# Performance work log

Hardware: AMD Instinct MI355X
Metric: run time of the kernel (lower is better)

## Reference

```python
import math
import jax, jax.numpy as jnp
import numpy as np

N = 50000       # num_nodes
D = 128         # input feature dim
OUT = 128       # output_dim
H = 8           # num_heads
F = OUT // H    # out_feats per head (= self_attn hidden_dim)
E_RAND = 800000 # random edges per graph (+ N self loops)
ALPHA = 0.8
BETA = 0.5


def _edges(key):
    k1, k2 = jax.random.split(key)
    src = jax.random.randint(k1, (E_RAND,), 0, N, dtype=jnp.int32)
    dst = jax.random.randint(k2, (E_RAND,), 0, N, dtype=jnp.int32)
    loop = jnp.arange(N, dtype=jnp.int32)  # dgl.add_self_loop
    return jnp.concatenate([src, loop]), jnp.concatenate([dst, loop])


def setup_inputs() -> dict:
    key = jax.random.key(0)
    ks = jax.random.split(key, 32)
    inp = {"x": jax.random.normal(ks[0], (N, D), jnp.float32)}
    inp["src_s"], inp["dst_s"] = _edges(ks[1])
    inp["src_t"], inp["dst_t"] = _edges(ks[2])
    inp["src_p"], inp["dst_p"] = _edges(ks[3])
    i = 4
    for v in ("s", "t", "p"):
        inp[f"W_{v}"] = jax.random.normal(ks[i], (OUT, D), jnp.float32) * 0.05; i += 1
        inp[f"al_{v}"] = jax.random.normal(ks[i], (H, F), jnp.float32) * 0.1; i += 1
        inp[f"ar_{v}"] = jax.random.normal(ks[i], (H, F), jnp.float32) * 0.1; i += 1
        inp[f"b_{v}"] = jnp.zeros((OUT,), jnp.float32)
    inp["Wq"] = jax.random.normal(ks[i], (F, OUT), jnp.float32) * 0.05; i += 1
    inp["bq"] = jnp.zeros((F,), jnp.float32)
    inp["Wk"] = jax.random.normal(ks[i], (F, OUT), jnp.float32) * 0.05; i += 1
    inp["bk"] = jnp.zeros((F,), jnp.float32)
    inp["Wm"] = jax.random.normal(ks[i], (1, N * OUT), jnp.float32) * 0.001; i += 1
    inp["bm"] = jnp.zeros((1,), jnp.float32)
    return inp


def _gat(x, src, dst, W, al, ar, b):
    # DGL GATConv (eval mode, negative_slope=0.2, activation=relu)
    feat = (x @ W.T).reshape(N, H, F)                      # [N,H,F]
    el = jnp.einsum('nhf,hf->nh', feat, al)                # [N,H]
    er = jnp.einsum('nhf,hf->nh', feat, ar)
    e = jax.nn.leaky_relu(el[src] + er[dst], 0.2)          # [E,H]
    m = jax.ops.segment_max(e, dst, num_segments=N)        # per-dst softmax
    ex = jnp.exp(e - m[dst])
    s = jax.ops.segment_sum(ex, dst, num_segments=N)
    attn = ex / s[dst]                                     # [E,H]
    out = jax.ops.segment_sum(feat[src] * attn[:, :, None], dst, num_segments=N)
    return jax.nn.relu(out + b.reshape(1, H, F)).reshape(N, OUT)


def reference(x, src_s, dst_s, src_t, dst_t, src_p, dst_p,
              W_s, al_s, ar_s, b_s, W_t, al_t, ar_t, b_t,
              W_p, al_p, ar_p, b_p, Wq, bq, Wk, bk, Wm, bm):
    s = _gat(x, src_s, dst_s, W_s, al_s, ar_s, b_s)
    t = _gat(x, src_t, dst_t, W_t, al_t, ar_t, b_t)
    p = _gat(x, src_p, dst_p, W_p, al_p, ar_p, b_p)
    views = jnp.stack([s, t, p])                           # [3,N,OUT]
    # self_attn: one scalar attention weight per view
    Q = jnp.einsum('vne,he->vnh', views, Wq) + bq          # [3,N,F]
    K = jnp.einsum('vne,he->vnh', views, Wk) + bk
    logits = jnp.sum(Q.reshape(3, -1) * K.reshape(3, -1), -1) / math.sqrt(F * N)
    w = jax.nn.softmax(logits)                             # [3]
    fused = w[:, None, None] * views
    views2 = ALPHA * fused + (1.0 - ALPHA) * views         # [3,N,OUT]
    # mv_attn: sigmoid-gated sum of views
    omega = jax.nn.sigmoid(views2.reshape(3, -1) @ Wm.T + bm)[:, 0]  # [3]
    mv = jnp.einsum('v,vne->ne', omega, views2)            # [N,OUT]
    result = BETA * views2 + (1.0 - BETA) * mv[None]       # [3,N,OUT]
    return mv, result
```

## Files before the change

kernel.cpp:

```cpp
#include <hip/hip_runtime.h>


#define N_NODES 50000
#define DIM 128
#define OUTD 128
#define NH 8
#define NF 16
#define NE 850000
#define NOFF 50001
#define NBUCK 49
#define BCAP 20480
#define BIN_EPT 8
#define BIN_EPB 2048

typedef float f32x4 __attribute__((ext_vector_type(4)));
typedef float f32x2 __attribute__((ext_vector_type(2)));
typedef __bf16 bf16x8 __attribute__((ext_vector_type(8)));
typedef unsigned short u16x8 __attribute__((ext_vector_type(8)));

static __device__ __forceinline__ float bf2f_lo(unsigned int u) {
  return __uint_as_float(u << 16);
}
static __device__ __forceinline__ float bf2f_hi(unsigned int u) {
  return __uint_as_float(u & 0xffff0000u);
}
static __device__ __forceinline__ f32x2 up2(unsigned int u) {
  f32x2 r;
  r.x = __uint_as_float(u << 16);
  r.y = __uint_as_float(u & 0xffff0000u);
  return r;
}
static __device__ __forceinline__ unsigned short f2bf(float f) {
  unsigned int u = __float_as_uint(f);
  unsigned int r = (u + 0x7fffu + ((u >> 16) & 1u)) >> 16;
  return (unsigned short)r;
}

__global__ __launch_bounds__(256) void gemm_feat_kernel(
    const float* __restrict__ x, const float* __restrict__ Ws,
    const float* __restrict__ Wt, const float* __restrict__ Wp,
    unsigned short* __restrict__ feat) {
  __shared__ unsigned short xa[128 * 128];
  __shared__ unsigned short wb[128 * 128];
  const int t = threadIdx.x;
  const int n0 = blockIdx.x * 128;

  for (int i = 0; i < 16; ++i) {
    int flat = (i * 256 + t) * 4;
    int r = flat >> 7, c = flat & 127;
    float4 val = make_float4(0.f, 0.f, 0.f, 0.f);
    if (n0 + r < N_NODES) val = *(const float4*)(x + (size_t)(n0 + r) * DIM + c);
    int byteoff = (r * 256 + c * 2) ^ ((r & 7) << 4);
    unsigned short* p = (unsigned short*)((char*)xa + byteoff);
    p[0] = f2bf(val.x); p[1] = f2bf(val.y); p[2] = f2bf(val.z); p[3] = f2bf(val.w);
  }

  const int wave = t >> 6, lane = t & 63;
  const int wr = wave >> 1, wc = wave & 1;
  const int lrow = lane & 15;
  const int kgrp = lane >> 4;

  for (int v = 0; v < 3; ++v) {
    const float* W = (v == 0) ? Ws : ((v == 1) ? Wt : Wp);
    __syncthreads();
    for (int i = 0; i < 16; ++i) {
      int flat = (i * 256 + t) * 4;
      int r = flat >> 7, c = flat & 127;
      float4 val = *(const float4*)(W + r * DIM + c);
      int byteoff = (r * 256 + c * 2) ^ ((r & 7) << 4);
      unsigned short* p = (unsigned short*)((char*)wb + byteoff);
      p[0] = f2bf(val.x); p[1] = f2bf(val.y); p[2] = f2bf(val.z); p[3] = f2bf(val.w);
    }
    __syncthreads();

    f32x4 acc[4][4];
    for (int m = 0; m < 4; ++m)
      for (int n = 0; n < 4; ++n) acc[m][n] = (f32x4)0.f;

    for (int ks = 0; ks < 4; ++ks) {
      bf16x8 af[4], bfr[4];
      int kb2 = (ks * 32 + kgrp * 8) * 2;
      for (int m = 0; m < 4; ++m) {
        int r = wr * 64 + m * 16 + lrow;
        af[m] = *(const bf16x8*)((const char*)xa + ((r * 256 + kb2) ^ ((r & 7) << 4)));
      }
      for (int n = 0; n < 4; ++n) {
        int r = wc * 64 + n * 16 + lrow;
        bfr[n] = *(const bf16x8*)((const char*)wb + ((r * 256 + kb2) ^ ((r & 7) << 4)));
      }
      for (int m = 0; m < 4; ++m)
        for (int n = 0; n < 4; ++n)
          acc[m][n] = __builtin_amdgcn_mfma_f32_16x16x32_bf16(af[m], bfr[n], acc[m][n], 0, 0, 0);
    }

    unsigned short* fv = feat + (size_t)v * N_NODES * OUTD;
    for (int m = 0; m < 4; ++m)
      for (int n = 0; n < 4; ++n) {
        int col = wc * 64 + n * 16 + lrow;
        for (int r4 = 0; r4 < 4; ++r4) {
          int row = n0 + wr * 64 + m * 16 + kgrp * 4 + r4;
          if (row < N_NODES) fv[(size_t)row * OUTD + col] = f2bf(acc[m][n][r4]);
        }
      }
  }
}

__global__ __launch_bounds__(256) void elr_kernel(
    const unsigned short* __restrict__ feat,
    const float* __restrict__ al_s, const float* __restrict__ ar_s,
    const float* __restrict__ al_t, const float* __restrict__ ar_t,
    const float* __restrict__ al_p, const float* __restrict__ ar_p,
    float* __restrict__ el, float* __restrict__ er) {
  int idx = blockIdx.x * 256 + threadIdx.x;
  if (idx >= 3 * N_NODES * NH) return;
  int v = idx / (N_NODES * NH);
  int rem = idx - v * (N_NODES * NH);
  int n = rem >> 3, h = rem & 7;
  const float* al = (v == 0) ? al_s : ((v == 1) ? al_t : al_p);
  const float* ar = (v == 0) ? ar_s : ((v == 1) ? ar_t : ar_p);
  const unsigned short* fr = feat + (size_t)v * N_NODES * OUTD + (size_t)n * OUTD + h * NF;
  uint4 a = *(const uint4*)(fr);
  uint4 b = *(const uint4*)(fr + 8);
  float fv[16];
  fv[0] = bf2f_lo(a.x); fv[1] = bf2f_hi(a.x); fv[2] = bf2f_lo(a.y); fv[3] = bf2f_hi(a.y);
  fv[4] = bf2f_lo(a.z); fv[5] = bf2f_hi(a.z); fv[6] = bf2f_lo(a.w); fv[7] = bf2f_hi(a.w);
  fv[8] = bf2f_lo(b.x); fv[9] = bf2f_hi(b.x); fv[10] = bf2f_lo(b.y); fv[11] = bf2f_hi(b.y);
  fv[12] = bf2f_lo(b.z); fv[13] = bf2f_hi(b.z); fv[14] = bf2f_lo(b.w); fv[15] = bf2f_hi(b.w);
  float accl = 0.f, accr = 0.f;
#pragma unroll
  for (int f = 0; f < NF; ++f) {
    accl += fv[f] * al[h * NF + f];
    accr += fv[f] * ar[h * NF + f];
  }
  el[idx] = accl;
  er[idx] = accr;
}

__global__ __launch_bounds__(256) void bin_kernel(
    const int* __restrict__ src_s, const int* __restrict__ dst_s,
    const int* __restrict__ src_t, const int* __restrict__ dst_t,
    const int* __restrict__ src_p, const int* __restrict__ dst_p,
    int* __restrict__ gtail, unsigned int* __restrict__ gbin) {
  const int v = blockIdx.y;
  const int* S = (v == 0) ? src_s : ((v == 1) ? src_t : src_p);
  const int* D = (v == 0) ? dst_s : ((v == 1) ? dst_t : dst_p);
  __shared__ int lhist[4][64], lbase[4][64];
  const int t = threadIdx.x;
  const int wave = t >> 6;
  ((int*)lhist)[t] = 0;
  __syncthreads();
  const int e0 = blockIdx.x * BIN_EPB + t * BIN_EPT;
  unsigned int pk[BIN_EPT];
  int bk[BIN_EPT], rk[BIN_EPT];
#pragma unroll
  for (int i = 0; i < BIN_EPT; ++i) {
    int e = e0 + i;
    if (e < NE) {
      unsigned int s = (unsigned int)S[e], d = (unsigned int)D[e];
      pk[i] = (s << 16) | d;
      bk[i] = (int)(d >> 10);
      rk[i] = atomicAdd(&lhist[wave][bk[i]], 1);
    } else {
      bk[i] = -1;
    }
  }
  __syncthreads();
  if (t < 64) {
    int c0 = lhist[0][t], c1 = lhist[1][t], c2 = lhist[2][t], c3 = lhist[3][t];
    int tot = c0 + c1 + c2 + c3;
    int gb = (tot > 0) ? atomicAdd(&gtail[v * 64 + t], tot) : 0;
    lbase[0][t] = gb;
    lbase[1][t] = gb + c0;
    lbase[2][t] = gb + c0 + c1;
    lbase[3][t] = gb + c0 + c1 + c2;
  }
  __syncthreads();
#pragma unroll
  for (int i = 0; i < BIN_EPT; ++i) {
    if (bk[i] >= 0) {
      int pos = lbase[wave][bk[i]] + rk[i];
      if (pos < BCAP)
        gbin[((size_t)v * 64 + bk[i]) * BCAP + pos] = pk[i];
    }
  }
}

__global__ __launch_bounds__(1024) void bucket_sort_kernel(
    const int* __restrict__ gtail, const unsigned int* __restrict__ gbin,
    int* __restrict__ offs, int* __restrict__ esrc) {
  __shared__ int lcur[1024];
  __shared__ int wsum[16];
  __shared__ int sh_bbase;
  __shared__ unsigned int sorted[BCAP];
  __shared__ int lhist[1024];
  const int v = blockIdx.y;
  const int b = blockIdx.x;
  const int t = threadIdx.x;
  const int wave = t >> 6, lane = t & 63;

  int cnt = gtail[v * 64 + b];
  if (cnt > BCAP) cnt = BCAP;
  const unsigned int* eb = gbin + ((size_t)v * 64 + b) * BCAP;

  if (t < 64) {
    int valb = (t < b) ? gtail[v * 64 + t] : 0;
#pragma unroll
    for (int m = 1; m < 64; m <<= 1) valb += __shfl_xor(valb, m, 64);
    if (t == 0) sh_bbase = valb;
  }
  lhist[t] = 0;
  __syncthreads();

  for (int e = t; e < cnt; e += 1024)
    atomicAdd(&lhist[eb[e] & 1023u], 1);
  __syncthreads();

  int val = lhist[t];
  int incl = val;
#pragma unroll
  for (int st = 1; st < 64; st <<= 1) {
    int o = __shfl_up(incl, st, 64);
    if (lane >= st) incl += o;
  }
  if (lane == 63) wsum[wave] = incl;
  __syncthreads();
  if (t < 64) {
    int wv = (lane < 16) ? wsum[lane] : 0;
    int winc = wv;
#pragma unroll
    for (int st = 1; st < 16; st <<= 1) {
      int o = __shfl_up(winc, st, 64);
      if (lane >= st) winc += o;
    }
    if (lane < 16) wsum[lane] = winc - wv;
  }
  __syncthreads();
  const int base = wsum[wave] + incl - val;
  lcur[t] = base;

  const int bbase = sh_bbase;
  if (b == 0 && t == 0) offs[v * NOFF] = 0;
  {
    int n = b * 1024 + t;
    if (n < N_NODES) offs[v * NOFF + n + 1] = bbase + base + val;
  }
  __syncthreads();

  for (int e = t; e < cnt; e += 1024) {
    unsigned int pk = eb[e];
    int pos = atomicAdd(&lcur[pk & 1023u], 1);
    sorted[pos] = pk >> 16;
  }
  __syncthreads();

  int* ev = esrc + (size_t)v * NE + bbase;
  for (int e = t; e < cnt; e += 1024) ev[e] = (int)sorted[e];
}

__global__ __launch_bounds__(256) void gat_kernel(
    const int* __restrict__ offs, const int* __restrict__ esrc,
    const float* __restrict__ el, const float* __restrict__ er,
    const unsigned short* __restrict__ feat,
    const float* __restrict__ b_s, const float* __restrict__ b_t,
    const float* __restrict__ b_p, float* __restrict__ views) {
  const int v = blockIdx.y;
  const int n = blockIdx.x * 4 + (threadIdx.x >> 6);
  const int lane = threadIdx.x & 63;
  const int g = lane >> 4;
  const int q = lane & 15;
  const int h = q >> 1;
  const int* off_v = offs + v * NOFF;
  const int off0 = off_v[n];
  const int deg = off_v[n + 1] - off0;
  const int* es = esrc + (size_t)v * NE + off0;
  const float* el_v = el + (size_t)v * N_NODES * NH;
  const float er_h = er[((size_t)v * N_NODES + n) * NH + h];
  const unsigned short* featv = feat + (size_t)v * N_NODES * OUTD;

  f32x2 acc2[4];
#pragma unroll
  for (int j = 0; j < 4; ++j) acc2[j] = (f32x2)0.f;
  float sm = 0.f;

  int e0 = g, e1 = 4 + g;
  bool v0 = e0 < deg, v1 = e1 < deg;
  int s0 = es[v0 ? e0 : 0];
  int s1 = es[v1 ? e1 : 0];
  float l0 = el_v[s0 * NH + h];
  float l1 = el_v[s1 * NH + h];
  uint4 pk0 = *(const uint4*)(featv + (size_t)s0 * OUTD + q * 8);
  uint4 pk1 = *(const uint4*)(featv + (size_t)s1 * OUTD + q * 8);

  for (int base = 0; base < deg; base += 8) {
    bool cv0 = v0, cv1 = v1;
    float cl0 = l0, cl1 = l1;
    uint4 cp0 = pk0, cp1 = pk1;
    int nb = base + 8;
    if (nb < deg) {
      e0 = nb + g; e1 = nb + 4 + g;
      v0 = e0 < deg; v1 = e1 < deg;
      s0 = es[v0 ? e0 : 0];
      s1 = es[v1 ? e1 : 0];
      l0 = el_v[s0 * NH + h];
      l1 = el_v[s1 * NH + h];
      pk0 = *(const uint4*)(featv + (size_t)s0 * OUTD + q * 8);
      pk1 = *(const uint4*)(featv + (size_t)s1 * OUTD + q * 8);
    }
    float val0 = cl0 + er_h;
    float val1 = cl1 + er_h;
    val0 = fmaxf(val0, 0.2f * val0);
    val1 = fmaxf(val1, 0.2f * val1);
    float aw0 = cv0 ? __expf(val0) : 0.f;
    float aw1 = cv1 ? __expf(val1) : 0.f;
    sm += aw0 + aw1;
    acc2[0] += aw0 * up2(cp0.x) + aw1 * up2(cp1.x);
    acc2[1] += aw0 * up2(cp0.y) + aw1 * up2(cp1.y);
    acc2[2] += aw0 * up2(cp0.z) + aw1 * up2(cp1.z);
    acc2[3] += aw0 * up2(cp0.w) + aw1 * up2(cp1.w);
  }

#pragma unroll
  for (int m = 16; m < 64; m <<= 1) {
    sm += __shfl_xor(sm, m, 64);
#pragma unroll
    for (int j = 0; j < 4; ++j) {
      acc2[j].x += __shfl_xor(acc2[j].x, m, 64);
      acc2[j].y += __shfl_xor(acc2[j].y, m, 64);
    }
  }

  if (g == 0) {
    const float inv = 1.0f / sm;
    const float* bv = (v == 0) ? b_s : ((v == 1) ? b_t : b_p);
    float r[8];
#pragma unroll
    for (int j = 0; j < 4; ++j) {
      float x0 = acc2[j].x * inv + bv[q * 8 + 2 * j];
      float x1 = acc2[j].y * inv + bv[q * 8 + 2 * j + 1];
      r[2 * j] = (x0 > 0.f) ? x0 : 0.f;
      r[2 * j + 1] = (x1 > 0.f) ? x1 : 0.f;
    }
    float* dst = views + (size_t)v * N_NODES * OUTD + (size_t)n * OUTD + q * 8;
    *(float4*)(dst) = make_float4(r[0], r[1], r[2], r[3]);
    *(float4*)(dst + 4) = make_float4(r[4], r[5], r[6], r[7]);
  }
}

__global__ __launch_bounds__(256) void viewred_kernel(
    const float* __restrict__ views, const float* __restrict__ Wq,
    const float* __restrict__ bq, const float* __restrict__ Wk,
    const float* __restrict__ bk, const float* __restrict__ Wm,
    float* __restrict__ logits, float* __restrict__ dsum) {
  __shared__ unsigned short vt[128 * 128];
  __shared__ unsigned short wq[16 * 128];
  __shared__ unsigned short wk[16 * 128];
  __shared__ float redq[4], redd[4];
  const int n0 = blockIdx.x * 128;
  const int t = threadIdx.x;
  const int wave = t >> 6, lane = t & 63;
  const int lrow = lane & 15;
  const int kgrp = lane >> 4;

  {
    int flat = t * 8;
    int r = flat >> 7, c = flat & 127;
    int byteoff = (r * 256 + c * 2) ^ ((r & 7) << 4);
    float4 qa = *(const float4*)(Wq + flat);
    float4 qb = *(const float4*)(Wq + flat + 4);
    u16x8 oq;
    oq[0] = f2bf(qa.x); oq[1] = f2bf(qa.y); oq[2] = f2bf(qa.z); oq[3] = f2bf(qa.w);
    oq[4] = f2bf(qb.x); oq[5] = f2bf(qb.y); oq[6] = f2bf(qb.z); oq[7] = f2bf(qb.w);
    *(u16x8*)((char*)wq + byteoff) = oq;
    float4 ka = *(const float4*)(Wk + flat);
    float4 kb = *(const float4*)(Wk + flat + 4);
    u16x8 ok;
    ok[0] = f2bf(ka.x); ok[1] = f2bf(ka.y); ok[2] = f2bf(ka.z); ok[3] = f2bf(ka.w);
    ok[4] = f2bf(kb.x); ok[5] = f2bf(kb.y); ok[6] = f2bf(kb.z); ok[7] = f2bf(kb.w);
    *(u16x8*)((char*)wk + byteoff) = ok;
  }

  const float bqv = bq[lrow];
  const float bkv = bk[lrow];

  for (int v = 0; v < 3; ++v) {
    const float* Vv = views + (size_t)v * N_NODES * OUTD;
    float dp = 0.f;
    for (int i = 0; i < 8; ++i) {
      int flat = (i * 256 + t) * 8;
      int r = flat >> 7, c = flat & 127;
      int row = n0 + r;
      u16x8 o = (u16x8)0;
      if (row < N_NODES) {
        size_t goff = (size_t)row * OUTD + c;
        float4 a = *(const float4*)(Vv + goff);
        float4 b = *(const float4*)(Vv + goff + 4);
        float4 wa = *(const float4*)(Wm + goff);
        float4 wb2 = *(const float4*)(Wm + goff + 4);
        dp += a.x * wa.x + a.y * wa.y + a.z * wa.z + a.w * wa.w;
        dp += b.x * wb2.x + b.y * wb2.y + b.z * wb2.z + b.w * wb2.w;
        o[0] = f2bf(a.x); o[1] = f2bf(a.y); o[2] = f2bf(a.z); o[3] = f2bf(a.w);
        o[4] = f2bf(b.x); o[5] = f2bf(b.y); o[6] = f2bf(b.z); o[7] = f2bf(b.w);
      }
      int byteoff = (r * 256 + c * 2) ^ ((r & 7) << 4);
      *(u16x8*)((char*)vt + byteoff) = o;
    }
    __syncthreads();

    float qk = 0.f;
    f32x4 accQ[2], accK[2];
    accQ[0] = (f32x4)0.f; accQ[1] = (f32x4)0.f;
    accK[0] = (f32x4)0.f; accK[1] = (f32x4)0.f;
    for (int ks = 0; ks < 4; ++ks) {
      int kb2 = (ks * 32 + kgrp * 8) * 2;
      int rb = lrow;
      bf16x8 bqf = *(const bf16x8*)((const char*)wq + ((rb * 256 + kb2) ^ ((rb & 7) << 4)));
      bf16x8 bkf = *(const bf16x8*)((const char*)wk + ((rb * 256 + kb2) ^ ((rb & 7) << 4)));
#pragma unroll
      for (int m = 0; m < 2; ++m) {
        int r = (wave * 2 + m) * 16 + lrow;
        bf16x8 af = *(const bf16x8*)((const char*)vt + ((r * 256 + kb2) ^ ((r & 7) << 4)));
        accQ[m] = __builtin_amdgcn_mfma_f32_16x16x32_bf16(af, bqf, accQ[m], 0, 0, 0);
        accK[m] = __builtin_amdgcn_mfma_f32_16x16x32_bf16(af, bkf, accK[m], 0, 0, 0);
      }
    }
#pragma unroll
    for (int m = 0; m < 2; ++m) {
#pragma unroll
      for (int j = 0; j < 4; ++j) {
        int row = n0 + (wave * 2 + m) * 16 + kgrp * 4 + j;
        if (row < N_NODES) qk += (accQ[m][j] + bqv) * (accK[m][j] + bkv);
      }
    }

#pragma unroll
    for (int m = 1; m < 64; m <<= 1) {
      qk += __shfl_xor(qk, m, 64);
      dp += __shfl_xor(dp, m, 64);
    }
    if (lane == 0) { redq[wave] = qk; redd[wave] = dp; }
    __syncthreads();
    if (t == 0) {
      atomicAdd(&logits[v], redq[0] + redq[1] + redq[2] + redq[3]);
      atomicAdd(&dsum[v], redd[0] + redd[1] + redd[2] + redd[3]);
    }
    __syncthreads();
  }
}

__global__ void scalar_kernel(const float* __restrict__ logits,
                              const float* __restrict__ dsum,
                              const float* __restrict__ bm, float* __restrict__ gc) {
  if (threadIdx.x == 0 && blockIdx.x == 0) {
    const float scale = 1.0f / sqrtf((float)(NF * N_NODES));
    float l0 = logits[0] * scale, l1 = logits[1] * scale, l2 = logits[2] * scale;
    float mx = fmaxf(l0, fmaxf(l1, l2));
    float e0 = __expf(l0 - mx), e1 = __expf(l1 - mx), e2 = __expf(l2 - mx);
    float inv = 1.0f / (e0 + e1 + e2);
    float g0 = 0.8f * e0 * inv + 0.2f;
    float g1 = 0.8f * e1 * inv + 0.2f;
    float g2 = 0.8f * e2 * inv + 0.2f;
    float bmv = bm[0];
    float o0 = 1.0f / (1.0f + __expf(-(g0 * dsum[0] + bmv)));
    float o1 = 1.0f / (1.0f + __expf(-(g1 * dsum[1] + bmv)));
    float o2 = 1.0f / (1.0f + __expf(-(g2 * dsum[2] + bmv)));
    gc[0] = g0; gc[1] = g1; gc[2] = g2;
    gc[3] = o0 * g0; gc[4] = o1 * g1; gc[5] = o2 * g2;
  }
}

__global__ __launch_bounds__(256) void final_kernel(
    const float* __restrict__ views, const float* __restrict__ gc,
    float* __restrict__ out) {
  const size_t NT = (size_t)N_NODES * OUTD;
  size_t base = ((size_t)blockIdx.x * 256 + threadIdx.x) * 4;
  if (base >= NT) return;
  float g0 = gc[0], g1 = gc[1], g2 = gc[2], c0 = gc[3], c1 = gc[4], c2 = gc[5];
  float4 a0 = *(const float4*)(views + base);
  float4 a1 = *(const float4*)(views + NT + base);
  float4 a2 = *(const float4*)(views + 2 * NT + base);
  float4 mv;
  mv.x = c0 * a0.x + c1 * a1.x + c2 * a2.x;
  mv.y = c0 * a0.y + c1 * a1.y + c2 * a2.y;
  mv.z = c0 * a0.z + c1 * a1.z + c2 * a2.z;
  mv.w = c0 * a0.w + c1 * a1.w + c2 * a2.w;
  *(float4*)(out + base) = mv;
  float4 r;
  r.x = 0.5f * (g0 * a0.x) + 0.5f * mv.x;
  r.y = 0.5f * (g0 * a0.y) + 0.5f * mv.y;
  r.z = 0.5f * (g0 * a0.z) + 0.5f * mv.z;
  r.w = 0.5f * (g0 * a0.w) + 0.5f * mv.w;
  *(float4*)(out + NT + base) = r;
  r.x = 0.5f * (g1 * a1.x) + 0.5f * mv.x;
  r.y = 0.5f * (g1 * a1.y) + 0.5f * mv.y;
  r.z = 0.5f * (g1 * a1.z) + 0.5f * mv.z;
  r.w = 0.5f * (g1 * a1.w) + 0.5f * mv.w;
  *(float4*)(out + 2 * NT + base) = r;
  r.x = 0.5f * (g2 * a2.x) + 0.5f * mv.x;
  r.y = 0.5f * (g2 * a2.y) + 0.5f * mv.y;
  r.z = 0.5f * (g2 * a2.z) + 0.5f * mv.z;
  r.w = 0.5f * (g2 * a2.w) + 0.5f * mv.w;
  *(float4*)(out + 3 * NT + base) = r;
}

extern "C" void kernel_launch(void* const* d_in, const int* in_sizes, int n_in,
                              void* d_out, int out_size, void* d_ws, size_t ws_size,
                              hipStream_t stream) {
  const float* x = (const float*)d_in[0];
  const int* src_s = (const int*)d_in[1];
  const int* dst_s = (const int*)d_in[2];
  const int* src_t = (const int*)d_in[3];
  const int* dst_t = (const int*)d_in[4];
  const int* src_p = (const int*)d_in[5];
  const int* dst_p = (const int*)d_in[6];
  const float* W_s = (const float*)d_in[7];
  const float* al_s = (const float*)d_in[8];
  const float* ar_s = (const float*)d_in[9];
  const float* b_s = (const float*)d_in[10];
  const float* W_t = (const float*)d_in[11];
  const float* al_t = (const float*)d_in[12];
  const float* ar_t = (const float*)d_in[13];
  const float* b_t = (const float*)d_in[14];
  const float* W_p = (const float*)d_in[15];
  const float* al_p = (const float*)d_in[16];
  const float* ar_p = (const float*)d_in[17];
  const float* b_p = (const float*)d_in[18];
  const float* Wq = (const float*)d_in[19];
  const float* bq = (const float*)d_in[20];
  const float* Wk = (const float*)d_in[21];
  const float* bk = (const float*)d_in[22];
  const float* Wm = (const float*)d_in[23];
  const float* bm = (const float*)d_in[24];
  float* out = (float*)d_out;

  char* ws = (char*)d_ws;
  unsigned short* feat = (unsigned short*)ws;
  float* el = (float*)(ws + 38400000);
  float* er = (float*)(ws + 43200000);
  float* views = (float*)(ws + 48000000);
  int* offs = (int*)(ws + 124800000);
  int* esrc = (int*)(ws + 126000016);
  int* gtail = (int*)(ws + 136800016);
  float* scal = (float*)(ws + 136800784);

  unsigned int* gbin = (unsigned int*)(ws + 49000000);

  hipMemsetAsync(gtail, 0, 768 + 48, stream);

  gemm_feat_kernel<<<dim3(391), dim3(256), 0, stream>>>(x, W_s, W_t, W_p, feat);
  elr_kernel<<<dim3((3 * N_NODES * NH + 255) / 256), dim3(256), 0, stream>>>(
      feat, al_s, ar_s, al_t, ar_t, al_p, ar_p, el, er);
  bin_kernel<<<dim3((NE + BIN_EPB - 1) / BIN_EPB, 3), dim3(256), 0, stream>>>(
      src_s, dst_s, src_t, dst_t, src_p, dst_p, gtail, gbin);
  bucket_sort_kernel<<<dim3(NBUCK, 3), dim3(1024), 0, stream>>>(
      gtail, gbin, offs, esrc);
  gat_kernel<<<dim3(12500, 3), dim3(256), 0, stream>>>(
      offs, esrc, el, er, feat, b_s, b_t, b_p, views);
  viewred_kernel<<<dim3(391), dim3(256), 0, stream>>>(
      views, Wq, bq, Wk, bk, Wm, scal, scal + 3);
  scalar_kernel<<<dim3(1), dim3(64), 0, stream>>>(scal, scal + 3, bm, scal + 6);
  final_kernel<<<dim3(6250), dim3(256), 0, stream>>>(views, scal + 6, out);
}
```

Before: 418.9 us.

## Fuse attention-score projection into GEMM, finer dst buckets, split view grid

The feature GEMM now runs one view per blockIdx.y and stages its bf16 tile in shared memory. From there it writes coalesced feat rows and computes el/er directly, so the separate elr kernel and its re-read of feat are gone. Edge binning uses 256-node buckets (196 buckets) with a separate scan kernel for bucket bases, and bucket sort scatters straight to global memory instead of staging in shared memory. The view-reduction kernel uses 64-row tiles with twice the blocks to raise parallelism. Smaller buckets could overflow BCAP under skewed degree distributions, and direct global scatter gives less coalesced writes.

```diff
diff --git a/kernel.cpp b/kernel.cpp
--- a/kernel.cpp
+++ b/kernel.cpp
@@ -8,10 +8,10 @@
 #define NF 16
 #define NE 850000
 #define NOFF 50001
-#define NBUCK 49
-#define BCAP 20480
-#define BIN_EPT 8
-#define BIN_EPB 2048
+#define NBUCK 196
+#define BCAP 5120
+#define BIN_EPT 16
+#define BIN_EPB 4096
 
 typedef float f32x4 __attribute__((ext_vector_type(4)));
 typedef float f32x2 __attribute__((ext_vector_type(2)));
@@ -20,9 +20,6 @@
 
 static __device__ __forceinline__ float bf2f_lo(unsigned int u) {
   return __uint_as_float(u << 16);
-}
-static __device__ __forceinline__ float bf2f_hi(unsigned int u) {
-  return __uint_as_float(u & 0xffff0000u);
 }
 static __device__ __forceinline__ f32x2 up2(unsigned int u) {
   f32x2 r;
@@ -39,11 +36,20 @@
 __global__ __launch_bounds__(256) void gemm_feat_kernel(
     const float* __restrict__ x, const float* __restrict__ Ws,
     const float* __restrict__ Wt, const float* __restrict__ Wp,
-    unsigned short* __restrict__ feat) {
+    const float* __restrict__ al_s, const float* __restrict__ ar_s,
+    const float* __restrict__ al_t, const float* __restrict__ ar_t,
+    const float* __restrict__ al_p, const float* __restrict__ ar_p,
+    unsigned short* __restrict__ feat, float* __restrict__ el,
+    float* __restrict__ er) {
   __shared__ unsigned short xa[128 * 128];
   __shared__ unsigned short wb[128 * 128];
+  __shared__ float alS[128], arS[128];
   const int t = threadIdx.x;
   const int n0 = blockIdx.x * 128;
+  const int v = blockIdx.y;
+  const float* W = (v == 0) ? Ws : ((v == 1) ? Wt : Wp);
+  const float* alv = (v == 0) ? al_s : ((v == 1) ? al_t : al_p);
+  const float* arv = (v == 0) ? ar_s : ((v == 1) ? ar_t : ar_p);
 
   for (int i = 0; i < 16; ++i) {
     int flat = (i * 256 + t) * 4;
@@ -54,86 +60,90 @@
     unsigned short* p = (unsigned short*)((char*)xa + byteoff);
     p[0] = f2bf(val.x); p[1] = f2bf(val.y); p[2] = f2bf(val.z); p[3] = f2bf(val.w);
   }
+  for (int i = 0; i < 16; ++i) {
+    int flat = (i * 256 + t) * 4;
+    int r = flat >> 7, c = flat & 127;
+    float4 val = *(const float4*)(W + r * DIM + c);
+    int byteoff = (r * 256 + c * 2) ^ ((r & 7) << 4);
+    unsigned short* p = (unsigned short*)((char*)wb + byteoff);
+    p[0] = f2bf(val.x); p[1] = f2bf(val.y); p[2] = f2bf(val.z); p[3] = f2bf(val.w);
+  }
+  if (t < 128) alS[t] = alv[t];
+  else arS[t - 128] = arv[t - 128];
+  __syncthreads();
 
   const int wave = t >> 6, lane = t & 63;
   const int wr = wave >> 1, wc = wave & 1;
   const int lrow = lane & 15;
   const int kgrp = lane >> 4;
-
-  for (int v = 0; v < 3; ++v) {
-    const float* W = (v == 0) ? Ws : ((v == 1) ? Wt : Wp);
-    __syncthreads();
-    for (int i = 0; i < 16; ++i) {
-      int flat = (i * 256 + t) * 4;
-      int r = flat >> 7, c = flat & 127;
-      float4 val = *(const float4*)(W + r * DIM + c);
-      int byteoff = (r * 256 + c * 2) ^ ((r & 7) << 4);
-      unsigned short* p = (unsigned short*)((char*)wb + byteoff);
-      p[0] = f2bf(val.x); p[1] = f2bf(val.y); p[2] = f2bf(val.z); p[3] = f2bf(val.w);
-    }
-    __syncthreads();
-
-    f32x4 acc[4][4];
+  const int row = t >> 1, half = t & 1;
+  const int grow = n0 + row;
+
+  f32x4 acc[4][4];
+  for (int m = 0; m < 4; ++m)
+    for (int n = 0; n < 4; ++n) acc[m][n] = (f32x4)0.f;
+
+  for (int ks = 0; ks < 4; ++ks) {
+    bf16x8 af[4], bfr[4];
+    int kb2 = (ks * 32 + kgrp * 8) * 2;
+    for (int m = 0; m < 4; ++m) {
+      int r = wr * 64 + m * 16 + lrow;
+      af[m] = *(const bf16x8*)((const char*)xa + ((r * 256 + kb2) ^ ((r & 7) << 4)));
+    }
+    for (int n = 0; n < 4; ++n) {
+      int r = wc * 64 + n * 16 + lrow;
+      bfr[n] = *(const bf16x8*)((const char*)wb + ((r * 256 + kb2) ^ ((r & 7) << 4)));
+    }
     for (int m = 0; m < 4; ++m)
-      for (int n = 0; n < 4; ++n) acc[m][n] = (f32x4)0.f;
-
-    for (int ks = 0; ks < 4; ++ks) {
-      bf16x8 af[4], bfr[4];
-      int kb2 = (ks * 32 + kgrp * 8) * 2;
-      for (int m = 0; m < 4; ++m) {
-        int r = wr * 64 + m * 16 + lrow;
-        af[m] = *(const bf16x8*)((const char*)xa + ((r * 256 + kb2) ^ ((r & 7) << 4)));
+      for (int n = 0; n < 4; ++n)
+        acc[m][n] = __builtin_amdgcn_mfma_f32_16x16x32_bf16(af[m], bfr[n], acc[m][n], 0, 0, 0);
+  }
+
+  __syncthreads();
+  for (int m = 0; m < 4; ++m)
+    for (int n = 0; n < 4; ++n) {
+      int col = wc * 64 + n * 16 + lrow;
+#pragma unroll
+      for (int r4 = 0; r4 < 4; ++r4) {
+        int r = wr * 64 + m * 16 + kgrp * 4 + r4;
+        int bo = (r * 256 + col * 2) ^ ((r & 7) << 4);
+        *(unsigned short*)((char*)wb + bo) = f2bf(acc[m][n][r4]);
       }
-      for (int n = 0; n < 4; ++n) {
-        int r = wc * 64 + n * 16 + lrow;
-        bfr[n] = *(const bf16x8*)((const char*)wb + ((r * 256 + kb2) ^ ((r & 7) << 4)));
+    }
+  __syncthreads();
+
+  unsigned short* fv = feat + (size_t)v * N_NODES * OUTD;
+  if (grow < N_NODES) {
+    const int cb = half * 64;
+#pragma unroll
+    for (int i = 0; i < 8; ++i) {
+      int c = cb + i * 8;
+      u16x8 val = *(const u16x8*)((const char*)wb + ((row * 256 + c * 2) ^ ((row & 7) << 4)));
+      *(u16x8*)(fv + (size_t)grow * OUTD + c) = val;
+    }
+    float4 elq, erq;
+    float* elp = (float*)&elq;
+    float* erp = (float*)&erq;
+#pragma unroll
+    for (int k = 0; k < 4; ++k) {
+      int h = half * 4 + k;
+      int c = h * 16;
+      u16x8 f0 = *(const u16x8*)((const char*)wb + ((row * 256 + c * 2) ^ ((row & 7) << 4)));
+      u16x8 f1 = *(const u16x8*)((const char*)wb + ((row * 256 + (c + 8) * 2) ^ ((row & 7) << 4)));
+      float accl = 0.f, accr = 0.f;
+#pragma unroll
+      for (int f = 0; f < 8; ++f) {
+        float v0 = bf2f_lo((unsigned int)(unsigned short)f0[f]);
+        float v1 = bf2f_lo((unsigned int)(unsigned short)f1[f]);
+        accl += v0 * alS[c + f] + v1 * alS[c + 8 + f];
+        accr += v0 * arS[c + f] + v1 * arS[c + 8 + f];
       }
-      for (int m = 0; m < 4; ++m)
-        for (int n = 0; n < 4; ++n)
-          acc[m][n] = __builtin_amdgcn_mfma_f32_16x16x32_bf16(af[m], bfr[n], acc[m][n], 0, 0, 0);
-    }
-
-    unsigned short* fv = feat + (size_t)v * N_NODES * OUTD;
-    for (int m = 0; m < 4; ++m)
-      for (int n = 0; n < 4; ++n) {
-        int col = wc * 64 + n * 16 + lrow;
-        for (int r4 = 0; r4 < 4; ++r4) {
-          int row = n0 + wr * 64 + m * 16 + kgrp * 4 + r4;
-          if (row < N_NODES) fv[(size_t)row * OUTD + col] = f2bf(acc[m][n][r4]);
-        }
-      }
-  }
-}
-
-__global__ __launch_bounds__(256) void elr_kernel(
-    const unsigned short* __restrict__ feat,
-    const float* __restrict__ al_s, const float* __restrict__ ar_s,
-    const float* __restrict__ al_t, const float* __restrict__ ar_t,
-    const float* __restrict__ al_p, const float* __restrict__ ar_p,
-    float* __restrict__ el, float* __restrict__ er) {
-  int idx = blockIdx.x * 256 + threadIdx.x;
-  if (idx >= 3 * N_NODES * NH) return;
-  int v = idx / (N_NODES * NH);
-  int rem = idx - v * (N_NODES * NH);
-  int n = rem >> 3, h = rem & 7;
-  const float* al = (v == 0) ? al_s : ((v == 1) ? al_t : al_p);
-  const float* ar = (v == 0) ? ar_s : ((v == 1) ? ar_t : ar_p);
-  const unsigned short* fr = feat + (size_t)v * N_NODES * OUTD + (size_t)n * OUTD + h * NF;
-  uint4 a = *(const uint4*)(fr);
-  uint4 b = *(const uint4*)(fr + 8);
-  float fv[16];
-  fv[0] = bf2f_lo(a.x); fv[1] = bf2f_hi(a.x); fv[2] = bf2f_lo(a.y); fv[3] = bf2f_hi(a.y);
-  fv[4] = bf2f_lo(a.z); fv[5] = bf2f_hi(a.z); fv[6] = bf2f_lo(a.w); fv[7] = bf2f_hi(a.w);
-  fv[8] = bf2f_lo(b.x); fv[9] = bf2f_hi(b.x); fv[10] = bf2f_lo(b.y); fv[11] = bf2f_hi(b.y);
-  fv[12] = bf2f_lo(b.z); fv[13] = bf2f_hi(b.z); fv[14] = bf2f_lo(b.w); fv[15] = bf2f_hi(b.w);
-  float accl = 0.f, accr = 0.f;
-#pragma unroll
-  for (int f = 0; f < NF; ++f) {
-    accl += fv[f] * al[h * NF + f];
-    accr += fv[f] * ar[h * NF + f];
-  }
-  el[idx] = accl;
-  er[idx] = accr;
+      elp[k] = accl; erp[k] = accr;
+    }
+    size_t eo = ((size_t)v * N_NODES + n0) * NH + t * 4;
+    *(float4*)(el + eo) = elq;
+    *(float4*)(er + eo) = erq;
+  }
 }
 
 __global__ __launch_bounds__(256) void bin_kernel(
@@ -144,31 +154,32 @@
   const int v = blockIdx.y;
   const int* S = (v == 0) ? src_s : ((v == 1) ? src_t : src_p);
   const int* D = (v == 0) ? dst_s : ((v == 1) ? dst_t : dst_p);
-  __shared__ int lhist[4][64], lbase[4][64];
+  __shared__ int lhist[4][256], lbase[4][256];
   const int t = threadIdx.x;
   const int wave = t >> 6;
-  ((int*)lhist)[t] = 0;
+#pragma unroll
+  for (int i = 0; i < 4; ++i) ((int*)lhist)[i * 256 + t] = 0;
   __syncthreads();
   const int e0 = blockIdx.x * BIN_EPB + t * BIN_EPT;
   unsigned int pk[BIN_EPT];
-  int bk[BIN_EPT], rk[BIN_EPT];
+  short bk[BIN_EPT], rk[BIN_EPT];
 #pragma unroll
   for (int i = 0; i < BIN_EPT; ++i) {
     int e = e0 + i;
     if (e < NE) {
       unsigned int s = (unsigned int)S[e], d = (unsigned int)D[e];
       pk[i] = (s << 16) | d;
-      bk[i] = (int)(d >> 10);
-      rk[i] = atomicAdd(&lhist[wave][bk[i]], 1);
+      bk[i] = (short)(d >> 8);
+      rk[i] = (short)atomicAdd(&lhist[wave][bk[i]], 1);
     } else {
       bk[i] = -1;
     }
   }
   __syncthreads();
-  if (t < 64) {
+  {
     int c0 = lhist[0][t], c1 = lhist[1][t], c2 = lhist[2][t], c3 = lhist[3][t];
     int tot = c0 + c1 + c2 + c3;
-    int gb = (tot > 0) ? atomicAdd(&gtail[v * 64 + t], tot) : 0;
+    int gb = (tot > 0) ? atomicAdd(&gtail[v * 256 + t], tot) : 0;
     lbase[0][t] = gb;
     lbase[1][t] = gb + c0;
     lbase[2][t] = gb + c0 + c1;
@@ -180,39 +191,58 @@
     if (bk[i] >= 0) {
       int pos = lbase[wave][bk[i]] + rk[i];
       if (pos < BCAP)
-        gbin[((size_t)v * 64 + bk[i]) * BCAP + pos] = pk[i];
-    }
-  }
-}
-
-__global__ __launch_bounds__(1024) void bucket_sort_kernel(
-    const int* __restrict__ gtail, const unsigned int* __restrict__ gbin,
+        gbin[((size_t)v * 256 + bk[i]) * BCAP + pos] = pk[i];
+    }
+  }
+}
+
+__global__ __launch_bounds__(256) void bscan_kernel(
+    const int* __restrict__ gtail, int* __restrict__ gbase) {
+  __shared__ int wsum[4];
+  const int t = threadIdx.x;
+  const int wave = t >> 6, lane = t & 63;
+  for (int v = 0; v < 3; ++v) {
+    int val = gtail[v * 256 + t];
+    if (val > BCAP) val = BCAP;
+    if (t >= NBUCK) val = 0;
+    int incl = val;
+#pragma unroll
+    for (int st = 1; st < 64; st <<= 1) {
+      int o = __shfl_up(incl, st, 64);
+      if (lane >= st) incl += o;
+    }
+    if (lane == 63) wsum[wave] = incl;
+    __syncthreads();
+    int wb = 0;
+#pragma unroll
+    for (int i = 0; i < 4; ++i) wb += (i < wave) ? wsum[i] : 0;
+    gbase[v * 256 + t] = wb + incl - val;
+    __syncthreads();
+  }
+}
+
+__global__ __launch_bounds__(256) void bucket_sort_kernel(
+    const int* __restrict__ gtail, const int* __restrict__ gbase,
+    const unsigned int* __restrict__ gbin,
     int* __restrict__ offs, int* __restrict__ esrc) {
-  __shared__ int lcur[1024];
-  __shared__ int wsum[16];
-  __shared__ int sh_bbase;
-  __shared__ unsigned int sorted[BCAP];
-  __shared__ int lhist[1024];
+  __shared__ int lhist[256];
+  __shared__ int lcur[256];
+  __shared__ int wsum[4];
   const int v = blockIdx.y;
   const int b = blockIdx.x;
   const int t = threadIdx.x;
   const int wave = t >> 6, lane = t & 63;
 
-  int cnt = gtail[v * 64 + b];
+  int cnt = gtail[v * 256 + b];
   if (cnt > BCAP) cnt = BCAP;
-  const unsigned int* eb = gbin + ((size_t)v * 64 + b) * BCAP;
-
-  if (t < 64) {
-    int valb = (t < b) ? gtail[v * 64 + t] : 0;
-#pragma unroll
-    for (int m = 1; m < 64; m <<= 1) valb += __shfl_xor(valb, m, 64);
-    if (t == 0) sh_bbase = valb;
-  }
+  const unsigned int* eb = gbin + ((size_t)v * 256 + b) * BCAP;
+  const int bbase = gbase[v * 256 + b];
+
   lhist[t] = 0;
   __syncthreads();
 
-  for (int e = t; e < cnt; e += 1024)
-    atomicAdd(&lhist[eb[e] & 1023u], 1);
+  for (int e = t; e < cnt; e += 256)
+    atomicAdd(&lhist[eb[e] & 255u], 1);
   __syncthreads();
 
   int val = lhist[t];
@@ -224,37 +254,25 @@
   }
   if (lane == 63) wsum[wave] = incl;
   __syncthreads();
-  if (t < 64) {
-    int wv = (lane < 16) ? wsum[lane] : 0;
-    int winc = wv;
-#pragma unroll
-    for (int st = 1; st < 16; st <<= 1) {
-      int o = __shfl_up(winc, st, 64);
-      if (lane >= st) winc += o;
-    }
-    if (lane < 16) wsum[lane] = winc - wv;
-  }
-  __syncthreads();
-  const int base = wsum[wave] + incl - val;
-  lcur[t] = base;
-
-  const int bbase = sh_bbase;
+  int wb = 0;
+#pragma unroll
+  for (int i = 0; i < 4; ++i) wb += (i < wave) ? wsum[i] : 0;
+  const int base = wb + incl - val;
+  lcur[t] = bbase + base;
+
   if (b == 0 && t == 0) offs[v * NOFF] = 0;
   {
-    int n = b * 1024 + t;
+    int n = b * 256 + t;
     if (n < N_NODES) offs[v * NOFF + n + 1] = bbase + base + val;
   }
   __syncthreads();
 
-  for (int e = t; e < cnt; e += 1024) {
+  int* ev = esrc + (size_t)v * NE;
+  for (int e = t; e < cnt; e += 256) {
     unsigned int pk = eb[e];
-    int pos = atomicAdd(&lcur[pk & 1023u], 1);
-    sorted[pos] = pk >> 16;
-  }
-  __syncthreads();
-
-  int* ev = esrc + (size_t)v * NE + bbase;
-  for (int e = t; e < cnt; e += 1024) ev[e] = (int)sorted[e];
+    int pos = atomicAdd(&lcur[pk & 255u], 1);
+    ev[pos] = (int)(pk >> 16);
+  }
 }
 
 __global__ __launch_bounds__(256) void gat_kernel(
@@ -340,7 +358,7 @@
       r[2 * j] = (x0 > 0.f) ? x0 : 0.f;
       r[2 * j + 1] = (x1 > 0.f) ? x1 : 0.f;
     }
-    float* dst = views + (size_t)v * N_NODES * OUTD + (size_t)n * OUTD + q * 8;
+    float* dst = views + ((size_t)v * N_NODES + n) * OUTD + q * 8;
     *(float4*)(dst) = make_float4(r[0], r[1], r[2], r[3]);
     *(float4*)(dst + 4) = make_float4(r[4], r[5], r[6], r[7]);
   }
@@ -351,11 +369,11 @@
     const float* __restrict__ bq, const float* __restrict__ Wk,
     const float* __restrict__ bk, const float* __restrict__ Wm,
     float* __restrict__ logits, float* __restrict__ dsum) {
-  __shared__ unsigned short vt[128 * 128];
+  __shared__ unsigned short vt[64 * 128];
   __shared__ unsigned short wq[16 * 128];
   __shared__ unsigned short wk[16 * 128];
   __shared__ float redq[4], redd[4];
-  const int n0 = blockIdx.x * 128;
+  const int n0 = blockIdx.x * 64;
   const int t = threadIdx.x;
   const int wave = t >> 6, lane = t & 63;
   const int lrow = lane & 15;
@@ -385,7 +403,7 @@
   for (int v = 0; v < 3; ++v) {
     const float* Vv = views + (size_t)v * N_NODES * OUTD;
     float dp = 0.f;
-    for (int i = 0; i < 8; ++i) {
+    for (int i = 0; i < 4; ++i) {
       int flat = (i * 256 + t) * 8;
       int r = flat >> 7, c = flat & 127;
       int row = n0 + r;
@@ -407,29 +425,21 @@
     __syncthreads();
 
     float qk = 0.f;
-    f32x4 accQ[2], accK[2];
-    accQ[0] = (f32x4)0.f; accQ[1] = (f32x4)0.f;
-    accK[0] = (f32x4)0.f; accK[1] = (f32x4)0.f;
+    f32x4 accQ = (f32x4)0.f, accK = (f32x4)0.f;
     for (int ks = 0; ks < 4; ++ks) {
       int kb2 = (ks * 32 + kgrp * 8) * 2;
       int rb = lrow;
       bf16x8 bqf = *(const bf16x8*)((const char*)wq + ((rb * 256 + kb2) ^ ((rb & 7) << 4)));
       bf16x8 bkf = *(const bf16x8*)((const char*)wk + ((rb * 256 + kb2) ^ ((rb & 7) << 4)));
-#pragma unroll
-      for (int m = 0; m < 2; ++m) {
-        int r = (wave * 2 + m) * 16 + lrow;
-        bf16x8 af = *(const bf16x8*)((const char*)vt + ((r * 256 + kb2) ^ ((r & 7) << 4)));
-        accQ[m] = __builtin_amdgcn_mfma_f32_16x16x32_bf16(af, bqf, accQ[m], 0, 0, 0);
-        accK[m] = __builtin_amdgcn_mfma_f32_16x16x32_bf16(af, bkf, accK[m], 0, 0, 0);
-      }
-    }
-#pragma unroll
-    for (int m = 0; m < 2; ++m) {
-#pragma unroll
-      for (int j = 0; j < 4; ++j) {
-        int row = n0 + (wave * 2 + m) * 16 + kgrp * 4 + j;
-        if (row < N_NODES) qk += (accQ[m][j] + bqv) * (accK[m][j] + bkv);
-      }
+      int r = wave * 16 + lrow;
+      bf16x8 af = *(const bf16x8*)((const char*)vt + ((r * 256 + kb2) ^ ((r & 7) << 4)));
+      accQ = __builtin_amdgcn_mfma_f32_16x16x32_bf16(af, bqf, accQ, 0, 0, 0);
+      accK = __builtin_amdgcn_mfma_f32_16x16x32_bf16(af, bkf, accK, 0, 0, 0);
+    }
+#pragma unroll
+    for (int j = 0; j < 4; ++j) {
+      int row = n0 + wave * 16 + kgrp * 4 + j;
+      if (row < N_NODES) qk += (accQ[j] + bqv) * (accK[j] + bkv);
     }
 
 #pragma unroll
@@ -540,22 +550,23 @@
   int* offs = (int*)(ws + 124800000);
   int* esrc = (int*)(ws + 126000016);
   int* gtail = (int*)(ws + 136800016);
-  float* scal = (float*)(ws + 136800784);
+  int* gbase = (int*)(ws + 136803088);
+  float* scal = (float*)(ws + 136806160);
 
   unsigned int* gbin = (unsigned int*)(ws + 49000000);
 
-  hipMemsetAsync(gtail, 0, 768 + 48, stream);
-
-  gemm_feat_kernel<<<dim3(391), dim3(256), 0, stream>>>(x, W_s, W_t, W_p, feat);
-  elr_kernel<<<dim3((3 * N_NODES * NH + 255) / 256), dim3(256), 0, stream>>>(
-      feat, al_s, ar_s, al_t, ar_t, al_p, ar_p, el, er);
+  hipMemsetAsync(gtail, 0, 3072 + 3072 + 48, stream);
+
+  gemm_feat_kernel<<<dim3(391, 3), dim3(256), 0, stream>>>(
+      x, W_s, W_t, W_p, al_s, ar_s, al_t, ar_t, al_p, ar_p, feat, el, er);
   bin_kernel<<<dim3((NE + BIN_EPB - 1) / BIN_EPB, 3), dim3(256), 0, stream>>>(
       src_s, dst_s, src_t, dst_t, src_p, dst_p, gtail, gbin);
-  bucket_sort_kernel<<<dim3(NBUCK, 3), dim3(1024), 0, stream>>>(
-      gtail, gbin, offs, esrc);
+  bscan_kernel<<<dim3(1), dim3(256), 0, stream>>>(gtail, gbase);
+  bucket_sort_kernel<<<dim3(NBUCK, 3), dim3(256), 0, stream>>>(
+      gtail, gbase, gbin, offs, esrc);
   gat_kernel<<<dim3(12500, 3), dim3(256), 0, stream>>>(
       offs, esrc, el, er, feat, b_s, b_t, b_p, views);
-  viewred_kernel<<<dim3(391), dim3(256), 0, stream>>>(
+  viewred_kernel<<<dim3(782), dim3(256), 0, stream>>>(
       views, Wq, bq, Wk, bk, Wm, scal, scal + 3);
   scalar_kernel<<<dim3(1), dim3(64), 0, stream>>>(scal, scal + 3, bm, scal + 6);
   final_kernel<<<dim3(6250), dim3(256), 0, stream>>>(views, scal + 6, out);
```

After: 468.3 us. 11.8% more time.
